# Performance work log

Hardware: AMD Instinct MI355X
Metric: run time of the kernel (lower is better)

The kernel has to match this reference:

```python
import jax, jax.numpy as jnp
import numpy as np
from jax import lax

B, N, G, K, D = 16, 8192, 256, 64, 256
DEPTH, H, HID, PH = 4, 8, 1024, 128
EPS = 1e-5
BN_SCALE = float(1.0 / np.sqrt(1.0 + 1e-5))  # BatchNorm eval, running mean 0 / var 1


def setup_inputs() -> dict:
    key = jax.random.key(0)
    ks = iter(jax.random.split(key, 48))
    def rn(shape, s=0.02):
        return jax.random.normal(next(ks), shape, jnp.float32) * s
    z = lambda *s: jnp.zeros(s, jnp.float32)
    o = lambda *s: jnp.ones(s, jnp.float32)
    return dict(
        x=jax.random.normal(next(ks), (B, N, 3), jnp.float32),
        enc_w1=rn((3, 128)), enc_b1=z(128), enc_bn1_g=o(128), enc_bn1_b=z(128),
        enc_w2=rn((128, 256)), enc_b2=z(256),
        enc_w3=rn((512, 512)), enc_b3=z(512), enc_bn2_g=o(512), enc_bn2_b=z(512),
        enc_w4=rn((512, D)), enc_b4=z(D),
        cls_token=rn((1, 1, D)), cls_pos=rn((1, 1, D)),
        pos_w1=rn((3, 128)), pos_b1=z(128), pos_w2=rn((128, D)), pos_b2=z(D),
        ln1_g=o(DEPTH, D), ln1_b=z(DEPTH, D),
        qkv_w=rn((DEPTH, D, 3 * D)),
        proj_w=rn((DEPTH, D, D)), proj_b=z(DEPTH, D),
        ln2_g=o(DEPTH, D), ln2_b=z(DEPTH, D),
        fc1_w=rn((DEPTH, D, HID)), fc1_b=z(DEPTH, HID),
        fc2_w=rn((DEPTH, HID, D)), fc2_b=z(DEPTH, D),
        norm_g=o(D), norm_b=z(D),
        head_w1=rn((D + 3, PH)), head_b1=z(PH), head_w2=rn((PH, 1)), head_b2=z(1),
    )


def layernorm(t, g, b):
    m = jnp.mean(t, -1, keepdims=True)
    v = jnp.mean((t - m) ** 2, -1, keepdims=True)
    return (t - m) / jnp.sqrt(v + EPS) * g + b


def fps(xyz, num_group):
    # farthest point sampling; deterministic start at index 0 (torch uses randint)
    Bb, Nn, _ = xyz.shape
    def body(i, st):
        dist, far, idxs = st
        idxs = idxs.at[:, i].set(far)
        cen = jnp.take_along_axis(xyz, far[:, None, None], axis=1)  # (B,1,3)
        d = jnp.sum((xyz - cen) ** 2, -1)
        dist = jnp.minimum(dist, d)
        far = jnp.argmax(dist, axis=1).astype(jnp.int32)
        return (dist, far, idxs)
    st0 = (jnp.full((Bb, Nn), 1e10, jnp.float32),
           jnp.zeros((Bb,), jnp.int32),
           jnp.zeros((Bb, num_group), jnp.int32))
    _, _, idxs = lax.fori_loop(0, num_group, body, st0)
    centers = jnp.take_along_axis(xyz, idxs[..., None], axis=1)  # (B,G,3)
    return centers, idxs


def knn(xyz, centers, k):
    # squared-distance cdist (same argsort order as p=2) + topk smallest
    c2 = jnp.sum(centers ** 2, -1)[:, :, None]
    x2 = jnp.sum(xyz ** 2, -1)[:, None, :]
    d2 = c2 + x2 - 2.0 * jnp.einsum('bgd,bnd->bgn', centers, xyz)  # (B,G,N)
    idx = lax.top_k(-d2, k)[1]  # (B,G,k)
    neigh = jax.vmap(lambda p, i: p[i])(xyz, idx)  # (B,G,k,3)
    return idx, neigh


def _forward(x, enc_w1, enc_b1, enc_bn1_g, enc_bn1_b, enc_w2, enc_b2,
             enc_w3, enc_b3, enc_bn2_g, enc_bn2_b, enc_w4, enc_b4,
             cls_token, cls_pos, pos_w1, pos_b1, pos_w2, pos_b2,
             ln1_g, ln1_b, qkv_w, proj_w, proj_b, ln2_g, ln2_b,
             fc1_w, fc1_b, fc2_w, fc2_b, norm_g, norm_b,
             head_w1, head_b1, head_w2, head_b2):
    Bb, Nn, _ = x.shape
    # grouping is @torch.no_grad() in the original -> stop_gradient
    pts = lax.stop_gradient(x)
    centers, _ = fps(pts, G)
    idx, neigh = knn(pts, centers, K)
    neigh = neigh - centers[:, :, None, :]  # (B,G,K,3) centered

    # PointNet encoder (kernel-size-1 convs == matmuls; BN eval with unit stats)
    pg = neigh.reshape(Bb * G, K, 3)
    h = pg @ enc_w1 + enc_b1                                # (BG,K,128)
    h = jax.nn.relu(h * enc_bn1_g * BN_SCALE + enc_bn1_b)
    h = h @ enc_w2 + enc_b2                                 # (BG,K,256)
    gmax = jnp.max(h, axis=1, keepdims=True)                # (BG,1,256)
    h = jnp.concatenate([jnp.broadcast_to(gmax, h.shape), h], -1)  # (BG,K,512)
    h = h @ enc_w3 + enc_b3
    h = jax.nn.relu(h * enc_bn2_g * BN_SCALE + enc_bn2_b)
    h = h @ enc_w4 + enc_b4                                 # (BG,K,D)
    tokens = jnp.max(h, axis=1).reshape(Bb, G, D)

    pos = jax.nn.gelu(centers @ pos_w1 + pos_b1, approximate=False) @ pos_w2 + pos_b2
    xt = jnp.concatenate([jnp.broadcast_to(cls_token, (Bb, 1, D)), tokens], 1)
    pt = jnp.concatenate([jnp.broadcast_to(cls_pos, (Bb, 1, D)), pos], 1)

    scale = (D // H) ** -0.5
    for l in range(DEPTH):
        xi = xt + pt  # pos added before every block
        h1 = layernorm(xi, ln1_g[l], ln1_b[l])
        qkv = (h1 @ qkv_w[l]).reshape(Bb, G + 1, 3, H, D // H).transpose(2, 0, 3, 1, 4)
        q, k_, v = qkv[0], qkv[1], qkv[2]
        attn = jax.nn.softmax(jnp.einsum('bhnd,bhmd->bhnm', q, k_) * scale, -1)
        o = jnp.einsum('bhnm,bhmd->bhnd', attn, v).transpose(0, 2, 1, 3).reshape(Bb, G + 1, D)
        xi = xi + o @ proj_w[l] + proj_b[l]
        h2 = layernorm(xi, ln2_g[l], ln2_b[l])
        xi = xi + jax.nn.gelu(h2 @ fc1_w[l] + fc1_b[l], approximate=False) @ fc2_w[l] + fc2_b[l]
        xt = xi
    xt = layernorm(xt, norm_g, norm_b)

    gfeat = xt[:, 1:, :]  # (B,G,D)
    concat = jnp.concatenate(
        [jnp.broadcast_to(gfeat[:, :, None, :], (Bb, G, K, D)), neigh], -1)  # (B,G,K,D+3)
    lg = (jax.nn.relu(concat @ head_w1 + head_b1) @ head_w2 + head_b2)[..., 0]  # (B,G,K)

    # scatter-mean per-point logits over original N points
    flat_i = idx.reshape(Bb, G * K)
    flat_v = lg.reshape(Bb, G * K)
    sums = jax.vmap(lambda v, i: jax.ops.segment_sum(v, i, num_segments=N))(flat_v, flat_i)
    cnts = jax.vmap(lambda i: jax.ops.segment_sum(jnp.ones(i.shape, jnp.float32), i, num_segments=N))(flat_i)
    return sums / jnp.maximum(cnts, 1.0)  # (B,N)


def reference(x, enc_w1, enc_b1, enc_bn1_g, enc_bn1_b, enc_w2, enc_b2,
              enc_w3, enc_b3, enc_bn2_g, enc_bn2_b, enc_w4, enc_b4,
              cls_token, cls_pos, pos_w1, pos_b1, pos_w2, pos_b2,
              ln1_g, ln1_b, qkv_w, proj_w, proj_b, ln2_g, ln2_b,
              fc1_w, fc1_b, fc2_w, fc2_b, norm_g, norm_b,
              head_w1, head_b1, head_w2, head_b2):
    return _forward(x, enc_w1, enc_b1, enc_bn1_g, enc_bn1_b, enc_w2, enc_b2,
                    enc_w3, enc_b3, enc_bn2_g, enc_bn2_b, enc_w4, enc_b4,
                    cls_token, cls_pos, pos_w1, pos_b1, pos_w2, pos_b2,
                    ln1_g, ln1_b, qkv_w, proj_w, proj_b, ln2_g, ln2_b,
                    fc1_w, fc1_b, fc2_w, fc2_b, norm_g, norm_b,
                    head_w1, head_b1, head_w2, head_b2)
```

## Files before the change

### kernel.cpp

```cpp
#include <hip/hip_runtime.h>
#include <hip/hip_bf16.h>

#define B_ 16
#define N_ 8192
#define G_ 256
#define K_ 64
#define D_ 256
#define HID_ 1024
#define EPS_ 1e-5f

typedef __attribute__((ext_vector_type(8))) short bf16x8;
typedef __attribute__((ext_vector_type(4))) float f32x4;

__device__ __forceinline__ float bf16_to_f32(unsigned short u){
  unsigned int v = ((unsigned int)u) << 16;
  return __uint_as_float(v);
}
__device__ __forceinline__ unsigned short f32_to_bf16(float f){
  unsigned int u = __float_as_uint(f);
  unsigned int r = (u + 0x7FFFu + ((u >> 16) & 1u)) >> 16;
  return (unsigned short)r;
}
__device__ __forceinline__ unsigned short bf16h(float a){
  __hip_bfloat16 h = __float2bfloat16(a);
  union { __hip_bfloat16 h; unsigned short u; } cv; cv.h = h; return cv.u;
}
__device__ __forceinline__ float gelu_exact(float v){
  return 0.5f * v * (1.0f + erff(v * 0.70710678118654752440f));
}

template<int CTRL>
__device__ __forceinline__ unsigned long long dpp64(unsigned long long k){
  int lo = (int)(unsigned int)k;
  int hi = (int)(unsigned int)(k >> 32);
  int dlo = __builtin_amdgcn_update_dpp(lo, lo, CTRL, 0xF, 0xF, false);
  int dhi = __builtin_amdgcn_update_dpp(hi, hi, CTRL, 0xF, 0xF, false);
  return (((unsigned long long)(unsigned int)dhi) << 32) | (unsigned int)dlo;
}
__device__ __forceinline__ unsigned long long bcast64(unsigned long long k, int lane){
  unsigned int lo = (unsigned int)__builtin_amdgcn_readlane((int)(unsigned int)k, lane);
  unsigned int hi = (unsigned int)__builtin_amdgcn_readlane((int)(unsigned int)(k >> 32), lane);
  return (((unsigned long long)hi) << 32) | lo;
}
__device__ __forceinline__ unsigned long long wave_max64(unsigned long long k){
  unsigned long long t;
  t = dpp64<0x111>(k); if (t > k) k = t;
  t = dpp64<0x112>(k); if (t > k) k = t;
  t = dpp64<0x114>(k); if (t > k) k = t;
  t = dpp64<0x118>(k); if (t > k) k = t;
  t = dpp64<0x142>(k); if (t > k) k = t;
  t = dpp64<0x143>(k); if (t > k) k = t;
  return bcast64(k, 63);
}
__device__ __forceinline__ unsigned long long wave_min64(unsigned long long k){
  unsigned long long t;
  t = dpp64<0x111>(k); if (t < k) k = t;
  t = dpp64<0x112>(k); if (t < k) k = t;
  t = dpp64<0x114>(k); if (t < k) k = t;
  t = dpp64<0x118>(k); if (t < k) k = t;
  t = dpp64<0x142>(k); if (t < k) k = t;
  t = dpp64<0x143>(k); if (t < k) k = t;
  return bcast64(k, 63);
}
__device__ __forceinline__ unsigned long long red8_max64(unsigned long long k){
  unsigned long long t;
  t = dpp64<0x111>(k); if (t > k) k = t;
  t = dpp64<0x112>(k); if (t > k) k = t;
  t = dpp64<0x114>(k); if (t > k) k = t;
  return bcast64(k, 7);
}
__device__ __forceinline__ unsigned long long red4_min64(unsigned long long k){
  unsigned long long t;
  t = dpp64<0x111>(k); if (t < k) k = t;
  t = dpp64<0x112>(k); if (t < k) k = t;
  return bcast64(k, 3);
}

__device__ __forceinline__ void packHi(const float* __restrict__ W, unsigned short* __restrict__ hi,
                                       int f, int N, int ksBits){
  int j = f & 7, lane = (f >> 3) & 63;
  int ks = (f >> 9) & ((1 << ksBits) - 1);
  int nt = f >> (9 + ksBits);
  int k = ks * 32 + ((lane >> 4) & 3) * 8 + j, c = nt * 16 + (lane & 15);
  hi[f] = f32_to_bf16(W[(size_t)k * N + c]);
}

__global__ __launch_bounds__(512) void prep_fps_kernel(
    const float* __restrict__ x, float* __restrict__ centers,
    const float* __restrict__ w1, const float* __restrict__ b1,
    const float* __restrict__ g1, const float* __restrict__ bb1,
    const float* __restrict__ w3, const float* __restrict__ b3,
    const float* __restrict__ g2, const float* __restrict__ bb2,
    const float* __restrict__ enc_w2, const float* __restrict__ enc_w4,
    const float* __restrict__ qkv_w, const float* __restrict__ proj_w,
    const float* __restrict__ fc1_w, const float* __restrict__ fc2_w,
    float* __restrict__ w1f, float* __restrict__ b1f, float* __restrict__ b3f,
    unsigned short* __restrict__ w2ph, unsigned short* __restrict__ w2pl,
    unsigned short* __restrict__ w3ph, unsigned short* __restrict__ w4ph,
    unsigned short* __restrict__ qkvPh, unsigned short* __restrict__ projPh,
    unsigned short* __restrict__ fc1Ph, unsigned short* __restrict__ fc2Ph,
    unsigned short* __restrict__ w3tp)
{
  const float S = 0.99999500003749968f;
  int blk = blockIdx.x, tid = threadIdx.x;

  if (blk >= 17){
    int f = (blk - 17) * 512 + tid;
    if (f < 32768){
      int j = f & 7, lane = (f >> 3) & 63, ks = (f >> 9) & 3, nt = f >> 11;
      int k = ks * 32 + ((lane >> 4) & 3) * 8 + j, c = nt * 16 + (lane & 15);
      float v = enc_w2[(size_t)k * 256 + c];
      unsigned short h = f32_to_bf16(v);
      w2ph[f] = h; w2pl[f] = f32_to_bf16(v - bf16_to_f32(h));
    } else if (f < 163840){
      f -= 32768;
      int j = f & 7, lane = (f >> 3) & 63, ks = (f >> 9) & 7, nt = f >> 12;
      int k = ks * 32 + ((lane >> 4) & 3) * 8 + j, c = nt * 16 + (lane & 15);
      w3ph[f] = f32_to_bf16(w3[(size_t)(256 + k) * 512 + c] * g2[c] * S);
    } else if (f < 294912){
      f -= 163840;
      packHi(enc_w4, w4ph, f, 256, 4);
    } else if (f < 1081344){
      f -= 294912;
      int l = f / 196608, fl = f - l * 196608;
      packHi(qkv_w + (size_t)l * 196608, qkvPh + (size_t)l * 196608, fl, 768, 3);
    } else if (f < 1343488){
      f -= 1081344;
      int l = f >> 16, fl = f & 65535;
      packHi(proj_w + (size_t)l * 65536, projPh + (size_t)l * 65536, fl, 256, 3);
    } else if (f < 2392064){
      f -= 1343488;
      int l = f >> 18, fl = f & 262143;
      packHi(fc1_w + (size_t)l * 262144, fc1Ph + (size_t)l * 262144, fl, 1024, 3);
    } else if (f < 3440640){
      f -= 2392064;
      int l = f >> 18, fl = f & 262143;
      packHi(fc2_w + (size_t)l * 262144, fc2Ph + (size_t)l * 262144, fl, 256, 5);
    } else {
      f -= 3440640;
      int j = f & 7, lane = (f >> 3) & 63, ks = (f >> 9) & 7, nt = f >> 12;
      int k = ks * 32 + ((lane >> 4) & 3) * 8 + j, c = nt * 16 + (lane & 15);
      w3tp[f] = f32_to_bf16(w3[(size_t)k * 512 + c] * g2[c] * S);
    }
    return;
  }
  if (blk == 16){
    if (tid < 384) w1f[tid] = w1[tid] * g1[tid & 127] * S;
    if (tid < 128) b1f[tid] = b1[tid] * g1[tid] * S + bb1[tid];
    b3f[tid] = b3[tid] * g2[tid] * S + bb2[tid];
    return;
  }

  int b = blk;
  const float* xb = x + (size_t)b * N_ * 3;
  int lane = tid & 63, wave = tid >> 6;
  float px[16], py[16], pz[16], dist[16];
#pragma unroll
  for (int j = 0; j < 16; j++){
    int p = tid + j * 512;
    px[j] = xb[p*3+0]; py[j] = xb[p*3+1]; pz[j] = xb[p*3+2];
    dist[j] = 1e10f;
  }
  __shared__ unsigned long long slotK[2][8];
  __shared__ float4 slotC[2][8];
  float cx = xb[0], cy = xb[1], cz = xb[2];
  for (int i = 0; i < G_; i++){
    if (tid == 0){
      float* cp = centers + ((size_t)b * G_ + i) * 3;
      cp[0] = cx; cp[1] = cy; cp[2] = cz;
    }
    float bestv = -1.0f; int bestj = 0;
#pragma unroll
    for (int j = 0; j < 16; j++){
      float dx = __fadd_rn(px[j], -cx);
      float dy = __fadd_rn(py[j], -cy);
      float dz = __fadd_rn(pz[j], -cz);
      float d  = __fadd_rn(__fadd_rn(__fmul_rn(dx,dx), __fmul_rn(dy,dy)), __fmul_rn(dz,dz));
      float dm = fminf(dist[j], d);
      dist[j] = dm;
      if (dm > bestv){ bestv = dm; bestj = j; }
    }
    unsigned int pid = (unsigned int)(tid + bestj * 512);
    unsigned long long key = (((unsigned long long)__float_as_uint(bestv)) << 32) | (unsigned long long)(~pid);
    key = wave_max64(key);
    int par = i & 1;
    unsigned int wpid = ~(unsigned int)key;
    if (lane == (int)(wpid & 63)){
      int jj = (int)(wpid >> 9);
      float fx = px[0], fy = py[0], fz = pz[0];
#pragma unroll
      for (int j = 1; j < 16; j++) if (jj == j){ fx = px[j]; fy = py[j]; fz = pz[j]; }
      slotK[par][wave] = key;
      slotC[par][wave] = make_float4(fx, fy, fz, 0.0f);
    }
    __syncthreads();
    if (i + 1 < G_){
      int sl = lane & 7;
      unsigned long long k2 = slotK[par][sl];
      float4 cc4 = slotC[par][sl];
      k2 = red8_max64(k2);
      unsigned int gpid = ~(unsigned int)k2;
      int s = (int)((gpid & 511u) >> 6);
      cx = __uint_as_float((unsigned int)__builtin_amdgcn_readlane((int)__float_as_uint(cc4.x), s));
      cy = __uint_as_float((unsigned int)__builtin_amdgcn_readlane((int)__float_as_uint(cc4.y), s));
      cz = __uint_as_float((unsigned int)__builtin_amdgcn_readlane((int)__float_as_uint(cc4.z), s));
    }
  }
}

__global__ __launch_bounds__(256) void knn_kernel(const float* __restrict__ x, const float* __restrict__ centers,
                                                  int* __restrict__ knn_idx, float* __restrict__ neigh)
{
  int blk = blockIdx.x, b = blk >> 8;
  const float* xb = x + (size_t)b * N_ * 3;
  const float* cc = centers + (size_t)blk * 3;
  int tid = threadIdx.x, lane = tid & 63, wave = tid >> 6;
  float c0 = cc[0], c1 = cc[1], c2v = cc[2];
  float c2s = __fadd_rn(__fadd_rn(__fmul_rn(c0,c0), __fmul_rn(c1,c1)), __fmul_rn(c2v,c2v));
  float d[32];
#pragma unroll
  for (int j = 0; j < 32; j++){
    int p = tid + j * 256;
    float x0 = xb[p*3+0], x1 = xb[p*3+1], x2 = xb[p*3+2];
    float xs = __fadd_rn(__fadd_rn(__fmul_rn(x0,x0), __fmul_rn(x1,x1)), __fmul_rn(x2,x2));
    float dt = __fadd_rn(__fadd_rn(__fmul_rn(c0,x0), __fmul_rn(c1,x1)), __fmul_rn(c2v,x2));
    d[j] = __fadd_rn(__fadd_rn(c2s, xs), -__fmul_rn(2.0f, dt));
  }
  const float FINF = __int_as_float(0x7F800000);
  float lmin = FINF; unsigned int lp = 0xFFFFFFFFu;
#pragma unroll
  for (int j = 0; j < 32; j++){ if (d[j] < lmin){ lmin = d[j]; lp = (unsigned int)(tid + j*256); } }
  __shared__ unsigned long long wred[2][4];
  for (int r = 0; r < K_; r++){
    unsigned int u = __float_as_uint(lmin);
    u = (u & 0x80000000u) ? ~u : (u | 0x80000000u);
    unsigned long long key = (((unsigned long long)u) << 32) | (unsigned long long)lp;
    key = wave_min64(key);
    int cur = r & 1;
    if (lane == 0) wred[cur][wave] = key;
    __syncthreads();
    unsigned long long m = red4_min64(wred[cur][lane & 3]);
    unsigned int p = (unsigned int)(m & 0xFFFFFFFFull);
    if (tid == (p & 255u)){
      knn_idx[(size_t)blk * K_ + r] = (int)p;
      float* np_ = neigh + ((size_t)blk * K_ + r) * 3;
      np_[0] = __fadd_rn(xb[p*3+0], -c0);
      np_[1] = __fadd_rn(xb[p*3+1], -c1);
      np_[2] = __fadd_rn(xb[p*3+2], -c2v);
      lmin = FINF; lp = 0xFFFFFFFFu;
#pragma unroll
      for (int j = 0; j < 32; j++){
        if ((unsigned int)(tid + j*256) == p) d[j] = FINF;
        if (d[j] < lmin){ lmin = d[j]; lp = (unsigned int)(tid + j*256); }
      }
    }
  }
}

__global__ __launch_bounds__(256, 2) void encoder_kernel(
    const float* __restrict__ neigh,
    const float* __restrict__ w1f, const float* __restrict__ b1f,
    const unsigned short* __restrict__ w2ph, const unsigned short* __restrict__ w2pl,
    const float* __restrict__ b2,
    const float* __restrict__ b3f,
    const unsigned short* __restrict__ w3ph, const unsigned short* __restrict__ w3tp,
    const unsigned short* __restrict__ w4ph,
    const float* __restrict__ b4,
    float* __restrict__ tokens)
{
  __shared__ __align__(16) unsigned short sH1[64 * 136];
  __shared__ __align__(16) unsigned short sH2[64 * 264];
  __shared__ __align__(16) float sShared[256];
  float (*sNeigh)[4] = (float(*)[4])sShared;
  unsigned short* sGmaxBf = (unsigned short*)sShared;

  int tid  = threadIdx.x;
  int wave = tid >> 6, lane = tid & 63, quad = lane >> 4, lrow = lane & 15;
  size_t gid = blockIdx.x;

  if (tid < 192) sNeigh[tid / 3][tid % 3] = neigh[gid * 192 + tid];
  __syncthreads();

  for (int e = tid; e < 8192; e += 256){
    int r = e >> 7, c = e & 127;
    float v = fmaf(sNeigh[r][2], w1f[256 + c], fmaf(sNeigh[r][1], w1f[128 + c], fmaf(sNeigh[r][0], w1f[c], b1f[c])));
    sH1[r * 136 + c] = bf16h(fmaxf(v, 0.0f));
  }
  __syncthreads();

  {
    f32x4 acc[4][4];
    const f32x4 z = {0.f, 0.f, 0.f, 0.f};
#pragma unroll
    for (int mt = 0; mt < 4; mt++)
#pragma unroll
      for (int nl = 0; nl < 4; nl++) acc[mt][nl] = z;
#pragma unroll
    for (int ks = 0; ks < 4; ks++){
      bf16x8 af[4];
#pragma unroll
      for (int mt = 0; mt < 4; mt++)
        af[mt] = *(const bf16x8*)&sH1[(mt*16 + lrow)*136 + ks*32 + quad*8];
#pragma unroll
      for (int nl = 0; nl < 4; nl++){
        size_t bo = (((size_t)(wave*4 + nl)*4 + ks)*64 + lane)*8;
        bf16x8 bh = *(const bf16x8*)&w2ph[bo];
        bf16x8 bl = *(const bf16x8*)&w2pl[bo];
#pragma unroll
        for (int mt = 0; mt < 4; mt++){
          acc[mt][nl] = __builtin_amdgcn_mfma_f32_16x16x32_bf16(af[mt], bh, acc[mt][nl], 0, 0, 0);
          acc[mt][nl] = __builtin_amdgcn_mfma_f32_16x16x32_bf16(af[mt], bl, acc[mt][nl], 0, 0, 0);
        }
      }
    }
#pragma unroll
    for (int nl = 0; nl < 4; nl++){
      int col = wave*64 + nl*16 + lrow;
      float bias = b2[col];
#pragma unroll
      for (int mt = 0; mt < 4; mt++)
#pragma unroll
        for (int rg = 0; rg < 4; rg++)
          sH2[(mt*16 + quad*4 + rg)*264 + col] = bf16h(acc[mt][nl][rg] + bias);
    }
  }
  __syncthreads();

  {
    float mx = -3.4e38f;
#pragma unroll 8
    for (int r = 0; r < 64; r++) mx = fmaxf(mx, bf16_to_f32(sH2[r*264 + tid]));
    sGmaxBf[tid] = bf16h(mx);
  }
  __syncthreads();

  f32x4 acc4[4][4];
  {
    const f32x4 z = {0.f, 0.f, 0.f, 0.f};
#pragma unroll
    for (int mt = 0; mt < 4; mt++)
#pragma unroll
      for (int nl = 0; nl < 4; nl++) acc4[mt][nl] = z;
  }
  for (int cc = 0; cc < 4; cc++){
    f32x4 acc3[4][2], accg[2];
    {
      const f32x4 z = {0.f, 0.f, 0.f, 0.f};
#pragma unroll
      for (int mt = 0; mt < 4; mt++){ acc3[mt][0] = z; acc3[mt][1] = z; }
      accg[0] = z; accg[1] = z;
    }
#pragma unroll
    for (int ks = 0; ks < 8; ks++){
      bf16x8 gf = *(const bf16x8*)&sGmaxBf[ks*32 + quad*8];
#pragma unroll
      for (int nl = 0; nl < 2; nl++){
        int nt = cc*8 + wave*2 + nl;
        size_t bo = (((size_t)nt*8 + ks)*64 + lane)*8;
        bf16x8 bh = *(const bf16x8*)&w3tp[bo];
        accg[nl] = __builtin_amdgcn_mfma_f32_16x16x32_bf16(gf, bh, accg[nl], 0, 0, 0);
      }
    }
#pragma unroll
    for (int ks = 0; ks < 8; ks++){
      bf16x8 af[4];
#pragma unroll
      for (int mt = 0; mt < 4; mt++)
        af[mt] = *(const bf16x8*)&sH2[(mt*16 + lrow)*264 + ks*32 + quad*8];
#pragma unroll
      for (int nl = 0; nl < 2; nl++){
        int nt = cc*8 + wave*2 + nl;
        size_t bo = (((size_t)nt*8 + ks)*64 + lane)*8;
        bf16x8 bh = *(const bf16x8*)&w3ph[bo];
#pragma unroll
        for (int mt = 0; mt < 4; mt++)
          acc3[mt][nl] = __builtin_amdgcn_mfma_f32_16x16x32_bf16(af[mt], bh, acc3[mt][nl], 0, 0, 0);
      }
    }
    __syncthreads();
#pragma unroll
    for (int nl = 0; nl < 2; nl++){
      int cl = wave*32 + nl*16 + lrow;
      int c  = cc*128 + cl;
      float bb = b3f[c];
#pragma unroll
      for (int mt = 0; mt < 4; mt++)
#pragma unroll
        for (int rg = 0; rg < 4; rg++)
          sH1[(mt*16 + quad*4 + rg)*136 + cl] = bf16h(fmaxf(acc3[mt][nl][rg] + accg[nl][rg] + bb, 0.0f));
    }
    __syncthreads();
#pragma unroll
    for (int ks = 0; ks < 4; ks++){
      bf16x8 af[4];
#pragma unroll
      for (int mt = 0; mt < 4; mt++)
        af[mt] = *(const bf16x8*)&sH1[(mt*16 + lrow)*136 + ks*32 + quad*8];
#pragma unroll
      for (int nl = 0; nl < 4; nl++){
        int nt = wave*4 + nl;
        size_t bo = (((size_t)nt*16 + cc*4 + ks)*64 + lane)*8;
        bf16x8 bh = *(const bf16x8*)&w4ph[bo];
#pragma unroll
        for (int mt = 0; mt < 4; mt++)
          acc4[mt][nl] = __builtin_amdgcn_mfma_f32_16x16x32_bf16(af[mt], bh, acc4[mt][nl], 0, 0, 0);
      }
    }
  }

#pragma unroll
  for (int nl = 0; nl < 4; nl++){
    float mx = -3.4e38f;
#pragma unroll
    for (int mt = 0; mt < 4; mt++)
#pragma unroll
      for (int rg = 0; rg < 4; rg++) mx = fmaxf(mx, acc4[mt][nl][rg]);
    mx = fmaxf(mx, __shfl_xor(mx, 16));
    mx = fmaxf(mx, __shfl_xor(mx, 32));
    if (quad == 0){
      int col = wave*64 + nl*16 + lrow;
      tokens[gid * 256 + col] = mx + b4[col];
    }
  }
}

__global__ __launch_bounds__(128) void pos_ln_kernel(
    const float* __restrict__ centers, const float* __restrict__ tokens,
    const float* __restrict__ cls_token, const float* __restrict__ cls_pos,
    const float* __restrict__ pw1, const float* __restrict__ pb1,
    const float* __restrict__ pw2, const float* __restrict__ pb2,
    const float* __restrict__ lng, const float* __restrict__ lnb,
    float* __restrict__ pt, float* __restrict__ xi, unsigned short* __restrict__ lnbuf)
{
  __shared__ float hS[128];
  __shared__ float red[2][2];
  int row = blockIdx.x;
  int b = row / 257, n = row - b * 257;
  int tid = threadIdx.x;
  size_t ro = (size_t)row * 256;
  float u0, u1;
  if (n == 0){
    float p0 = cls_pos[tid], p1 = cls_pos[128 + tid];
    u0 = cls_token[tid] + p0; u1 = cls_token[128 + tid] + p1;
    pt[ro + tid] = p0; pt[ro + 128 + tid] = p1;
  } else {
    int g = n - 1;
    const float* c = centers + ((size_t)b * 256 + g) * 3;
    float h = fmaf(c[2], pw1[256 + tid], fmaf(c[1], pw1[128 + tid], fmaf(c[0], pw1[tid], pb1[tid])));
    hS[tid] = gelu_exact(h);
    __syncthreads();
    const float* tok = tokens + ((size_t)b * 256 + g) * 256;
    float s0 = pb2[tid], s1 = pb2[128 + tid];
#pragma unroll 4
    for (int k = 0; k < 128; k++){
      s0 = fmaf(hS[k], pw2[(size_t)k * 256 + tid], s0);
      s1 = fmaf(hS[k], pw2[(size_t)k * 256 + 128 + tid], s1);
    }
    pt[ro + tid] = s0; pt[ro + 128 + tid] = s1;
    u0 = tok[tid] + s0; u1 = tok[128 + tid] + s1;
  }
  float s = u0 + u1, q = u0*u0 + u1*u1;
#pragma unroll
  for (int o = 32; o; o >>= 1){ s += __shfl_down(s, o); q += __shfl_down(q, o); }
  int wv = tid >> 6;
  if ((tid & 63) == 0){ red[0][wv] = s; red[1][wv] = q; }
  __syncthreads();
  float m  = (red[0][0] + red[0][1]) * (1.0f / 256.0f);
  float var = (red[1][0] + red[1][1]) * (1.0f / 256.0f) - m * m;
  float rs = 1.0f / sqrtf(var + EPS_);
  xi[ro + tid] = u0; xi[ro + 128 + tid] = u1;
  lnbuf[ro + tid] = bf16h((u0 - m) * rs * lng[tid] + lnb[tid]);
  lnbuf[ro + 128 + tid] = bf16h((u1 - m) * rs * lng[128 + tid] + lnb[128 + tid]);
}

template<int ACT>
__global__ __launch_bounds__(256) void mfma_gemm(
    const unsigned short* __restrict__ A, const unsigned short* __restrict__ Bh,
    const float* __restrict__ bias, unsigned short* __restrict__ C, int M, int K, int N)
{
  __shared__ __align__(16) unsigned short sA[64 * 72];
  int tid = threadIdx.x;
  int wave = tid >> 6, lane = tid & 63, quad = lane >> 4, lrow = lane & 15;
  int row0 = blockIdx.x * 64;
  int col0 = blockIdx.y * 128;
  int ksTotal = K >> 5;
  f32x4 acc[4][2];
  const f32x4 z = {0.f, 0.f, 0.f, 0.f};
#pragma unroll
  for (int mt = 0; mt < 4; mt++){ acc[mt][0] = z; acc[mt][1] = z; }

  for (int k0 = 0; k0 < K; k0 += 64){
#pragma unroll
    for (int i = 0; i < 2; i++){
      int e = tid + i * 256;
      int r = e >> 3, c8 = (e & 7) * 8;
      int gr = row0 + r;
      bf16x8 v = {0,0,0,0,0,0,0,0};
      if (gr < M) v = *(const bf16x8*)(A + (size_t)gr * K + k0 + c8);
      *(bf16x8*)&sA[r * 72 + c8] = v;
    }
    __syncthreads();
    int ksBase = k0 >> 5;
#pragma unroll
    for (int ks = 0; ks < 2; ks++){
      bf16x8 af[4];
#pragma unroll
      for (int mt = 0; mt < 4; mt++)
        af[mt] = *(const bf16x8*)&sA[(mt*16 + lrow)*72 + ks*32 + quad*8];
#pragma unroll
      for (int nl = 0; nl < 2; nl++){
        int nt = (col0 >> 4) + wave*2 + nl;
        size_t bo = (((size_t)nt * ksTotal + ksBase + ks)*64 + lane)*8;
        bf16x8 bh = *(const bf16x8*)&Bh[bo];
#pragma unroll
        for (int mt = 0; mt < 4; mt++)
          acc[mt][nl] = __builtin_amdgcn_mfma_f32_16x16x32_bf16(af[mt], bh, acc[mt][nl], 0, 0, 0);
      }
    }
    __syncthreads();
  }
#pragma unroll
  for (int nl = 0; nl < 2; nl++){
    int c = col0 + wave*32 + nl*16 + lrow;
    float bc = bias ? bias[c] : 0.0f;
#pragma unroll
    for (int mt = 0; mt < 4; mt++)
#pragma unroll
      for (int rg = 0; rg < 4; rg++){
        int r = row0 + mt*16 + quad*4 + rg;
        if (r < M){
          float v = acc[mt][nl][rg] + bc;
          if (ACT == 1) v = gelu_exact(v);
          C[(size_t)r * N + c] = bf16h(v);
        }
      }
  }
}

__global__ __launch_bounds__(256) void mfma_gemm_ln(
    const unsigned short* __restrict__ A, const unsigned short* __restrict__ Bh,
    const float* __restrict__ bias, const float* __restrict__ res,
    const float* __restrict__ ptb,
    float* __restrict__ C, float* __restrict__ xiOut, unsigned short* __restrict__ lnOut,
    const float* __restrict__ lng, const float* __restrict__ lnb, int M, int K)
{
  __shared__ __align__(16) unsigned short sA[64 * 72];
  __shared__ float sRed[2][64][4];
  int tid = threadIdx.x;
  int wave = tid >> 6, lane = tid & 63, quad = lane >> 4, lrow = lane & 15;
  int row0 = blockIdx.x * 64;
  int ksTotal = K >> 5;
  f32x4 acc[4][4];
  const f32x4 z = {0.f, 0.f, 0.f, 0.f};
#pragma unroll
  for (int mt = 0; mt < 4; mt++)
#pragma unroll
    for (int nl = 0; nl < 4; nl++) acc[mt][nl] = z;

  for (int k0 = 0; k0 < K; k0 += 64){
#pragma unroll
    for (int i = 0; i < 2; i++){
      int e = tid + i * 256;
      int r = e >> 3, c8 = (e & 7) * 8;
      int gr = row0 + r;
      bf16x8 v = {0,0,0,0,0,0,0,0};
      if (gr < M) v = *(const bf16x8*)(A + (size_t)gr * K + k0 + c8);
      *(bf16x8*)&sA[r * 72 + c8] = v;
    }
    __syncthreads();
    int ksBase = k0 >> 5;
#pragma unroll
    for (int ks = 0; ks < 2; ks++){
      bf16x8 af[4];
#pragma unroll
      for (int mt = 0; mt < 4; mt++)
        af[mt] = *(const bf16x8*)&sA[(mt*16 + lrow)*72 + ks*32 + quad*8];
#pragma unroll
      for (int nl = 0; nl < 4; nl++){
        int nt = wave*4 + nl;
        size_t bo = (((size_t)nt * ksTotal + ksBase + ks)*64 + lane)*8;
        bf16x8 bh = *(const bf16x8*)&Bh[bo];
#pragma unroll
        for (int mt = 0; mt < 4; mt++)
          acc[mt][nl] = __builtin_amdgcn_mfma_f32_16x16x32_bf16(af[mt], bh, acc[mt][nl], 0, 0, 0);
      }
    }
    __syncthreads();
  }
#pragma unroll
  for (int nl = 0; nl < 4; nl++){
    int c = wave*64 + nl*16 + lrow;
    float bc = bias[c];
#pragma unroll
    for (int mt = 0; mt < 4; mt++)
#pragma unroll
      for (int rg = 0; rg < 4; rg++){
        int r = row0 + mt*16 + quad*4 + rg;
        if (r < M){
          float v = acc[mt][nl][rg] + bc + res[(size_t)r * 256 + c];
          if (C) C[(size_t)r * 256 + c] = v;
          float u = v;
          if (ptb) u += ptb[(size_t)r * 256 + c];
          acc[mt][nl][rg] = u;
        }
      }
  }
#pragma unroll
  for (int mt = 0; mt < 4; mt++)
#pragma unroll
    for (int rg = 0; rg < 4; rg++){
      int rloc = mt*16 + quad*4 + rg;
      float s = 0.0f, q = 0.0f;
#pragma unroll
      for (int nl = 0; nl < 4; nl++){ float u = acc[mt][nl][rg]; s += u; q += u*u; }
#pragma unroll
      for (int off = 1; off < 16; off <<= 1){ s += __shfl_xor(s, off); q += __shfl_xor(q, off); }
      if (lrow == 0){ sRed[0][rloc][wave] = s; sRed[1][rloc][wave] = q; }
    }
  __syncthreads();
#pragma unroll
  for (int mt = 0; mt < 4; mt++)
#pragma unroll
    for (int rg = 0; rg < 4; rg++){
      int rloc = mt*16 + quad*4 + rg;
      int r = row0 + rloc;
      if (r >= M) continue;
      float s = ((sRed[0][rloc][0] + sRed[0][rloc][1]) + sRed[0][rloc][2]) + sRed[0][rloc][3];
      float q = ((sRed[1][rloc][0] + sRed[1][rloc][1]) + sRed[1][rloc][2]) + sRed[1][rloc][3];
      float m  = s * (1.0f / 256.0f);
      float var = q * (1.0f / 256.0f) - m * m;
      float rs = 1.0f / sqrtf(var + EPS_);
#pragma unroll
      for (int nl = 0; nl < 4; nl++){
        int c = wave*64 + nl*16 + lrow;
        float u = acc[mt][nl][rg];
        lnOut[(size_t)r * 256 + c] = bf16h((u - m) * rs * lng[c] + lnb[c]);
        if (xiOut) xiOut[(size_t)r * 256 + c] = u;
      }
    }
}

__global__ __launch_bounds__(256) void attn_kernel(const unsigned short* __restrict__ qkv, unsigned short* __restrict__ obuf)
{
  int bh = blockIdx.x;
  int b = bh >> 3, h = bh & 7;
  int tid = threadIdx.x;
  int qi = tid >> 2, kp = tid & 3;
  int qrow = blockIdx.y * 64 + qi;
  bool act = qrow < 257;
  __shared__ float kS[128][33];
  __shared__ float vS[128][33];
  const unsigned short* qb = qkv + (size_t)b * 257 * 768;
  float q[32], o[32];
  float mrun = -3.4e38f, l = 0.0f;
  if (act){
    const unsigned short* qr = qb + (size_t)qrow * 768 + h * 32;
#pragma unroll
    for (int j = 0; j < 32; j++){ q[j] = bf16_to_f32(qr[j]); o[j] = 0.0f; }
  }
  const float scale = 0.17677669529663687f;
  for (int m0 = 0; m0 < 257; m0 += 128){
    int cnt = min(128, 257 - m0);
    for (int e = tid; e < cnt * 32; e += 256){
      int mm = e >> 5, j = e & 31;
      const unsigned short* rowp = qb + (size_t)(m0 + mm) * 768 + h * 32;
      kS[mm][j] = bf16_to_f32(rowp[256 + j]);
      vS[mm][j] = bf16_to_f32(rowp[512 + j]);
    }
    __syncthreads();
    if (act){
      for (int mm = kp; mm < cnt; mm += 4){
        float s = 0.0f;
#pragma unroll
        for (int j = 0; j < 32; j++) s = fmaf(q[j], kS[mm][j], s);
        s *= scale;
        float nm = fmaxf(mrun, s);
        float alpha = expf(mrun - nm);
        float p = expf(s - nm);
        l = fmaf(l, alpha, p);
#pragma unroll
        for (int j = 0; j < 32; j++) o[j] = fmaf(p, vS[mm][j], o[j] * alpha);
        mrun = nm;
      }
    }
    __syncthreads();
  }
  if (act){
#pragma unroll
    for (int msk = 1; msk <= 2; msk <<= 1){
      float m2 = __shfl_xor(mrun, msk);
      float l2 = __shfl_xor(l, msk);
      float nm = fmaxf(mrun, m2);
      float a1 = expf(mrun - nm), a2 = expf(m2 - nm);
      l = l * a1 + l2 * a2;
#pragma unroll
      for (int j = 0; j < 32; j++){
        float o2 = __shfl_xor(o[j], msk);
        o[j] = o[j] * a1 + o2 * a2;
      }
      mrun = nm;
    }
    if (kp == 0){
      float inv = 1.0f / l;
      unsigned short* orow = obuf + (size_t)(b * 257 + qrow) * 256 + h * 32;
#pragma unroll
      for (int j = 0; j < 32; j++) orow[j] = bf16h(o[j] * inv);
    }
  }
}

__global__ __launch_bounds__(256) void head_kernel(
    const unsigned short* __restrict__ gfeat, const float* __restrict__ neigh, const int* __restrict__ knn_idx,
    const float* __restrict__ w1, const float* __restrict__ b1,
    const float* __restrict__ w2, const float* __restrict__ b2,
    float* __restrict__ sums, float* __restrict__ cnts)
{
  int blk = blockIdx.x, b = blk >> 8;
  __shared__ float xS[256];
  __shared__ float nS[64][4];
  __shared__ float partH[2][128];
  __shared__ float sharedH[128];
  __shared__ float w2S[128];
  __shared__ float wtail[3][128];
  int tid = threadIdx.x;
  xS[tid] = bf16_to_f32(gfeat[((size_t)b * 257 + 1 + (blk & 255)) * 256 + tid]);
  if (tid < 192) nS[tid / 3][tid % 3] = neigh[(size_t)blk * 192 + tid];
  if (tid < 128){
    w2S[tid] = w2[tid];
    wtail[0][tid] = w1[256 * 128 + tid];
    wtail[1][tid] = w1[257 * 128 + tid];
    wtail[2][tid] = w1[258 * 128 + tid];
  }
  __syncthreads();
  {
    int half = tid >> 7, j = tid & 127;
    float s = 0.0f;
#pragma unroll 8
    for (int k = 0; k < 128; k++) s = fmaf(xS[half * 128 + k], w1[(size_t)(half * 128 + k) * 128 + j], s);
    partH[half][j] = s;
  }
  __syncthreads();
  if (tid < 128) sharedH[tid] = partH[0][tid] + partH[1][tid] + b1[tid];
  __syncthreads();
  int r = tid >> 2, q = tid & 3;
  float n0 = nS[r][0], n1 = nS[r][1], n2 = nS[r][2];
  float s = 0.0f;
#pragma unroll
  for (int j0 = 0; j0 < 32; j0++){
    int j = q * 32 + j0;
    float h = fmaf(n2, wtail[2][j], fmaf(n1, wtail[1][j], fmaf(n0, wtail[0][j], sharedH[j])));
    s = fmaf(fmaxf(h, 0.0f), w2S[j], s);
  }
  s += __shfl_xor(s, 1);
  s += __shfl_xor(s, 2);
  if (q == 0){
    float lg = s + b2[0];
    int p = knn_idx[(size_t)blk * K_ + r];
    atomicAdd(&sums[(size_t)b * N_ + p], lg);
    atomicAdd(&cnts[(size_t)b * N_ + p], 1.0f);
  }
}

__global__ void finalize_kernel(const float* __restrict__ sums, const float* __restrict__ cnts, float* __restrict__ out)
{
  int i = blockIdx.x * 256 + threadIdx.x;
  out[i] = sums[i] / fmaxf(cnts[i], 1.0f);
}

extern "C" void kernel_launch(void* const* d_in, const int* in_sizes, int n_in,
                              void* d_out, int out_size, void* d_ws, size_t ws_size,
                              hipStream_t stream)
{
  (void)in_sizes; (void)n_in; (void)out_size; (void)ws_size;
  const float* x        = (const float*)d_in[0];
  const float* enc_w1   = (const float*)d_in[1];
  const float* enc_b1   = (const float*)d_in[2];
  const float* enc_bn1g = (const float*)d_in[3];
  const float* enc_bn1b = (const float*)d_in[4];
  const float* enc_w2   = (const float*)d_in[5];
  const float* enc_b2   = (const float*)d_in[6];
  const float* enc_w3   = (const float*)d_in[7];
  const float* enc_b3   = (const float*)d_in[8];
  const float* enc_bn2g = (const float*)d_in[9];
  const float* enc_bn2b = (const float*)d_in[10];
  const float* enc_w4   = (const float*)d_in[11];
  const float* enc_b4   = (const float*)d_in[12];
  const float* cls_tok  = (const float*)d_in[13];
  const float* cls_pos  = (const float*)d_in[14];
  const float* pos_w1   = (const float*)d_in[15];
  const float* pos_b1   = (const float*)d_in[16];
  const float* pos_w2   = (const float*)d_in[17];
  const float* pos_b2   = (const float*)d_in[18];
  const float* ln1_g    = (const float*)d_in[19];
  const float* ln1_b    = (const float*)d_in[20];
  const float* qkv_w    = (const float*)d_in[21];
  const float* proj_w   = (const float*)d_in[22];
  const float* proj_b   = (const float*)d_in[23];
  const float* ln2_g    = (const float*)d_in[24];
  const float* ln2_b    = (const float*)d_in[25];
  const float* fc1_w    = (const float*)d_in[26];
  const float* fc1_b    = (const float*)d_in[27];
  const float* fc2_w    = (const float*)d_in[28];
  const float* fc2_b    = (const float*)d_in[29];
  const float* norm_g   = (const float*)d_in[30];
  const float* norm_b   = (const float*)d_in[31];
  const float* head_w1  = (const float*)d_in[32];
  const float* head_b1  = (const float*)d_in[33];
  const float* head_w2  = (const float*)d_in[34];
  const float* head_b2  = (const float*)d_in[35];

  float* ws = (float*)d_ws;
  size_t off = 0;
  auto alloc = [&](size_t n)->float*{ float* p = ws + off; off += (n + 63) & ~(size_t)63; return p; };

  float* centers = alloc((size_t)B_ * G_ * 3);
  float* w1f     = alloc(384);
  float* b1f     = alloc(128);
  float* b3f     = alloc(512);
  unsigned short* w2ph = (unsigned short*)alloc(16384);
  unsigned short* w2pl = (unsigned short*)alloc(16384);
  unsigned short* w3ph = (unsigned short*)alloc(65536);
  unsigned short* w3tp = (unsigned short*)alloc(65536);
  unsigned short* w4ph = (unsigned short*)alloc(65536);
  unsigned short* qkvPh = (unsigned short*)alloc(393216);
  unsigned short* projPh = (unsigned short*)alloc(131072);
  unsigned short* fc1Ph = (unsigned short*)alloc(524288);
  unsigned short* fc2Ph = (unsigned short*)alloc(524288);
  float* tokens  = alloc((size_t)B_ * G_ * D_);
  float* neigh   = alloc((size_t)B_ * G_ * K_ * 3);
  int*   knn_idx = (int*)alloc((size_t)B_ * G_ * K_);
  float* pt      = alloc((size_t)B_ * 257 * D_);
  float* xi      = alloc((size_t)B_ * 257 * D_);
  unsigned short* lnbufB = (unsigned short*)alloc((size_t)B_ * 257 * D_ / 2 + 64);
  unsigned short* obufB  = (unsigned short*)alloc((size_t)B_ * 257 * D_ / 2 + 64);
  unsigned short* bigbufB= (unsigned short*)alloc((size_t)B_ * 257 * HID_ / 2 + 64);
  unsigned short* gfeatB = (unsigned short*)alloc((size_t)B_ * 257 * D_ / 2 + 64);
  float* sums    = alloc((size_t)B_ * N_);
  float* cnts    = alloc((size_t)B_ * N_);

  hipMemsetAsync(sums, 0, (size_t)2 * B_ * N_ * sizeof(float), stream);

  prep_fps_kernel<<<6993, 512, 0, stream>>>(x, centers,
      enc_w1, enc_b1, enc_bn1g, enc_bn1b, enc_w3, enc_b3, enc_bn2g, enc_bn2b,
      enc_w2, enc_w4, qkv_w, proj_w, fc1_w, fc2_w,
      w1f, b1f, b3f, w2ph, w2pl, w3ph, w4ph, qkvPh, projPh, fc1Ph, fc2Ph, w3tp);

  knn_kernel<<<B_ * G_, 256, 0, stream>>>(x, centers, knn_idx, neigh);
  encoder_kernel<<<B_ * G_, 256, 0, stream>>>(neigh, w1f, b1f, w2ph, w2pl, enc_b2,
                                              b3f, w3ph, w3tp, w4ph, enc_b4, tokens);
  pos_ln_kernel<<<B_ * 257, 128, 0, stream>>>(centers, tokens, cls_tok, cls_pos,
                                              pos_w1, pos_b1, pos_w2, pos_b2,
                                              ln1_g, ln1_b, pt, xi, lnbufB);
  const int M = B_ * 257;
  for (int l = 0; l < 4; l++){
    mfma_gemm<0><<<dim3(65, 6), 256, 0, stream>>>(lnbufB, qkvPh + (size_t)l*196608, nullptr, bigbufB, M, 256, 768);
    attn_kernel<<<dim3(B_ * 8, 5), 256, 0, stream>>>(bigbufB, obufB);
    mfma_gemm_ln<<<65, 256, 0, stream>>>(obufB, projPh + (size_t)l*65536, proj_b + l*256, xi, nullptr,
                                         xi, nullptr, lnbufB, ln2_g + l*256, ln2_b + l*256, M, 256);
    mfma_gemm<1><<<dim3(65, 8), 256, 0, stream>>>(lnbufB, fc1Ph + (size_t)l*262144, fc1_b + l*1024, bigbufB, M, 256, 1024);
    if (l < 3){
      mfma_gemm_ln<<<65, 256, 0, stream>>>(bigbufB, fc2Ph + (size_t)l*262144, fc2_b + l*256, xi, pt,
                                           nullptr, xi, lnbufB, ln1_g + (l+1)*256, ln1_b + (l+1)*256, M, 1024);
    } else {
      mfma_gemm_ln<<<65, 256, 0, stream>>>(bigbufB, fc2Ph + (size_t)l*262144, fc2_b + l*256, xi, nullptr,
                                           nullptr, nullptr, gfeatB, norm_g, norm_b, M, 1024);
    }
  }
  head_kernel<<<B_ * G_, 256, 0, stream>>>(gfeatB, neigh, knn_idx, head_w1, head_b1, head_w2, head_b2, sums, cnts);
  finalize_kernel<<<(B_ * N_) / 256, 256, 0, stream>>>(sums, cnts, (float*)d_out);
}
```

Baseline: 1.814 ms.

## Buffer FPS/KNN outputs in LDS and shrink GEMM row tiles for more blocks

FPS centers and KNN indices/neighbour offsets are now staged in shared memory and written to global memory in one coalesced pass at kernel end, instead of scattered single-thread stores inside the serial loops. The transformer GEMMs shrink their row tile from 64 to 32 rows (plain GEMM) and to 16 rows (GEMM+LayerNorm), which multiplies the grid size so the M≈4112 problem fills more compute units. The smaller tiles reduce weight reuse per block and increase redundant B-operand loads.

```diff
diff --git a/kernel.cpp b/kernel.cpp
--- a/kernel.cpp
+++ b/kernel.cpp
@@ -163,11 +163,11 @@
   }
   __shared__ unsigned long long slotK[2][8];
   __shared__ float4 slotC[2][8];
+  __shared__ float sCen[G_ * 3];
   float cx = xb[0], cy = xb[1], cz = xb[2];
   for (int i = 0; i < G_; i++){
     if (tid == 0){
-      float* cp = centers + ((size_t)b * G_ + i) * 3;
-      cp[0] = cx; cp[1] = cy; cp[2] = cz;
+      sCen[i*3+0] = cx; sCen[i*3+1] = cy; sCen[i*3+2] = cz;
     }
     float bestv = -1.0f; int bestj = 0;
 #pragma unroll
@@ -206,6 +206,9 @@
       cz = __uint_as_float((unsigned int)__builtin_amdgcn_readlane((int)__float_as_uint(cc4.z), s));
     }
   }
+  __syncthreads();
+  for (int e = tid; e < G_ * 3; e += 512)
+    centers[(size_t)b * G_ * 3 + e] = sCen[e];
 }
 
 __global__ __launch_bounds__(256) void knn_kernel(const float* __restrict__ x, const float* __restrict__ centers,
@@ -231,6 +234,8 @@
 #pragma unroll
   for (int j = 0; j < 32; j++){ if (d[j] < lmin){ lmin = d[j]; lp = (unsigned int)(tid + j*256); } }
   __shared__ unsigned long long wred[2][4];
+  __shared__ int sIdx[K_];
+  __shared__ float sNei[K_ * 3];
   for (int r = 0; r < K_; r++){
     unsigned int u = __float_as_uint(lmin);
     u = (u & 0x80000000u) ? ~u : (u | 0x80000000u);
@@ -242,11 +247,10 @@
     unsigned long long m = red4_min64(wred[cur][lane & 3]);
     unsigned int p = (unsigned int)(m & 0xFFFFFFFFull);
     if (tid == (p & 255u)){
-      knn_idx[(size_t)blk * K_ + r] = (int)p;
-      float* np_ = neigh + ((size_t)blk * K_ + r) * 3;
-      np_[0] = __fadd_rn(xb[p*3+0], -c0);
-      np_[1] = __fadd_rn(xb[p*3+1], -c1);
-      np_[2] = __fadd_rn(xb[p*3+2], -c2v);
+      sIdx[r] = (int)p;
+      sNei[r*3+0] = __fadd_rn(xb[p*3+0], -c0);
+      sNei[r*3+1] = __fadd_rn(xb[p*3+1], -c1);
+      sNei[r*3+2] = __fadd_rn(xb[p*3+2], -c2v);
       lmin = FINF; lp = 0xFFFFFFFFu;
 #pragma unroll
       for (int j = 0; j < 32; j++){
@@ -255,6 +259,9 @@
       }
     }
   }
+  __syncthreads();
+  if (tid < K_) knn_idx[(size_t)blk * K_ + tid] = sIdx[tid];
+  if (tid < K_ * 3) neigh[(size_t)blk * K_ * 3 + tid] = sNei[tid];
 }
 
 __global__ __launch_bounds__(256, 2) void encoder_kernel(
@@ -478,22 +485,20 @@
     const unsigned short* __restrict__ A, const unsigned short* __restrict__ Bh,
     const float* __restrict__ bias, unsigned short* __restrict__ C, int M, int K, int N)
 {
-  __shared__ __align__(16) unsigned short sA[64 * 72];
+  __shared__ __align__(16) unsigned short sA[32 * 72];
   int tid = threadIdx.x;
   int wave = tid >> 6, lane = tid & 63, quad = lane >> 4, lrow = lane & 15;
-  int row0 = blockIdx.x * 64;
+  int row0 = blockIdx.x * 32;
   int col0 = blockIdx.y * 128;
   int ksTotal = K >> 5;
-  f32x4 acc[4][2];
+  f32x4 acc[2][2];
   const f32x4 z = {0.f, 0.f, 0.f, 0.f};
 #pragma unroll
-  for (int mt = 0; mt < 4; mt++){ acc[mt][0] = z; acc[mt][1] = z; }
+  for (int mt = 0; mt < 2; mt++){ acc[mt][0] = z; acc[mt][1] = z; }
 
   for (int k0 = 0; k0 < K; k0 += 64){
-#pragma unroll
-    for (int i = 0; i < 2; i++){
-      int e = tid + i * 256;
-      int r = e >> 3, c8 = (e & 7) * 8;
+    {
+      int r = tid >> 3, c8 = (tid & 7) * 8;
       int gr = row0 + r;
       bf16x8 v = {0,0,0,0,0,0,0,0};
       if (gr < M) v = *(const bf16x8*)(A + (size_t)gr * K + k0 + c8);
@@ -503,9 +508,9 @@
     int ksBase = k0 >> 5;
 #pragma unroll
     for (int ks = 0; ks < 2; ks++){
-      bf16x8 af[4];
-#pragma unroll
-      for (int mt = 0; mt < 4; mt++)
+      bf16x8 af[2];
+#pragma unroll
+      for (int mt = 0; mt < 2; mt++)
         af[mt] = *(const bf16x8*)&sA[(mt*16 + lrow)*72 + ks*32 + quad*8];
 #pragma unroll
       for (int nl = 0; nl < 2; nl++){
@@ -513,7 +518,7 @@
         size_t bo = (((size_t)nt * ksTotal + ksBase + ks)*64 + lane)*8;
         bf16x8 bh = *(const bf16x8*)&Bh[bo];
 #pragma unroll
-        for (int mt = 0; mt < 4; mt++)
+        for (int mt = 0; mt < 2; mt++)
           acc[mt][nl] = __builtin_amdgcn_mfma_f32_16x16x32_bf16(af[mt], bh, acc[mt][nl], 0, 0, 0);
       }
     }
@@ -524,7 +529,7 @@
     int c = col0 + wave*32 + nl*16 + lrow;
     float bc = bias ? bias[c] : 0.0f;
 #pragma unroll
-    for (int mt = 0; mt < 4; mt++)
+    for (int mt = 0; mt < 2; mt++)
 #pragma unroll
       for (int rg = 0; rg < 4; rg++){
         int r = row0 + mt*16 + quad*4 + rg;
@@ -544,24 +549,20 @@
     float* __restrict__ C, float* __restrict__ xiOut, unsigned short* __restrict__ lnOut,
     const float* __restrict__ lng, const float* __restrict__ lnb, int M, int K)
 {
-  __shared__ __align__(16) unsigned short sA[64 * 72];
-  __shared__ float sRed[2][64][4];
+  __shared__ __align__(16) unsigned short sA[16 * 72];
+  __shared__ float sRed[2][16][4];
   int tid = threadIdx.x;
   int wave = tid >> 6, lane = tid & 63, quad = lane >> 4, lrow = lane & 15;
-  int row0 = blockIdx.x * 64;
+  int row0 = blockIdx.x * 16;
   int ksTotal = K >> 5;
-  f32x4 acc[4][4];
+  f32x4 acc[4];
   const f32x4 z = {0.f, 0.f, 0.f, 0.f};
 #pragma unroll
-  for (int mt = 0; mt < 4; mt++)
-#pragma unroll
-    for (int nl = 0; nl < 4; nl++) acc[mt][nl] = z;
+  for (int nl = 0; nl < 4; nl++) acc[nl] = z;
 
   for (int k0 = 0; k0 < K; k0 += 64){
-#pragma unroll
-    for (int i = 0; i < 2; i++){
-      int e = tid + i * 256;
-      int r = e >> 3, c8 = (e & 7) * 8;
+    if (tid < 128){
+      int r = tid >> 3, c8 = (tid & 7) * 8;
       int gr = row0 + r;
       bf16x8 v = {0,0,0,0,0,0,0,0};
       if (gr < M) v = *(const bf16x8*)(A + (size_t)gr * K + k0 + c8);
@@ -571,18 +572,13 @@
     int ksBase = k0 >> 5;
 #pragma unroll
     for (int ks = 0; ks < 2; ks++){
-      bf16x8 af[4];
-#pragma unroll
-      for (int mt = 0; mt < 4; mt++)
-        af[mt] = *(const bf16x8*)&sA[(mt*16 + lrow)*72 + ks*32 + quad*8];
+      bf16x8 af = *(const bf16x8*)&sA[lrow*72 + ks*32 + quad*8];
 #pragma unroll
       for (int nl = 0; nl < 4; nl++){
         int nt = wave*4 + nl;
         size_t bo = (((size_t)nt * ksTotal + ksBase + ks)*64 + lane)*8;
         bf16x8 bh = *(const bf16x8*)&Bh[bo];
-#pragma unroll
-        for (int mt = 0; mt < 4; mt++)
-          acc[mt][nl] = __builtin_amdgcn_mfma_f32_16x16x32_bf16(af[mt], bh, acc[mt][nl], 0, 0, 0);
+        acc[nl] = __builtin_amdgcn_mfma_f32_16x16x32_bf16(af, bh, acc[nl], 0, 0, 0);
       }
     }
     __syncthreads();
@@ -592,52 +588,46 @@
     int c = wave*64 + nl*16 + lrow;
     float bc = bias[c];
 #pragma unroll
-    for (int mt = 0; mt < 4; mt++)
-#pragma unroll
-      for (int rg = 0; rg < 4; rg++){
-        int r = row0 + mt*16 + quad*4 + rg;
-        if (r < M){
-          float v = acc[mt][nl][rg] + bc + res[(size_t)r * 256 + c];
-          if (C) C[(size_t)r * 256 + c] = v;
-          float u = v;
-          if (ptb) u += ptb[(size_t)r * 256 + c];
-          acc[mt][nl][rg] = u;
-        }
-      }
-  }
-#pragma unroll
-  for (int mt = 0; mt < 4; mt++)
-#pragma unroll
     for (int rg = 0; rg < 4; rg++){
-      int rloc = mt*16 + quad*4 + rg;
-      float s = 0.0f, q = 0.0f;
-#pragma unroll
-      for (int nl = 0; nl < 4; nl++){ float u = acc[mt][nl][rg]; s += u; q += u*u; }
-#pragma unroll
-      for (int off = 1; off < 16; off <<= 1){ s += __shfl_xor(s, off); q += __shfl_xor(q, off); }
-      if (lrow == 0){ sRed[0][rloc][wave] = s; sRed[1][rloc][wave] = q; }
-    }
-  __syncthreads();
-#pragma unroll
-  for (int mt = 0; mt < 4; mt++)
-#pragma unroll
-    for (int rg = 0; rg < 4; rg++){
-      int rloc = mt*16 + quad*4 + rg;
-      int r = row0 + rloc;
-      if (r >= M) continue;
-      float s = ((sRed[0][rloc][0] + sRed[0][rloc][1]) + sRed[0][rloc][2]) + sRed[0][rloc][3];
-      float q = ((sRed[1][rloc][0] + sRed[1][rloc][1]) + sRed[1][rloc][2]) + sRed[1][rloc][3];
-      float m  = s * (1.0f / 256.0f);
-      float var = q * (1.0f / 256.0f) - m * m;
-      float rs = 1.0f / sqrtf(var + EPS_);
-#pragma unroll
-      for (int nl = 0; nl < 4; nl++){
-        int c = wave*64 + nl*16 + lrow;
-        float u = acc[mt][nl][rg];
-        lnOut[(size_t)r * 256 + c] = bf16h((u - m) * rs * lng[c] + lnb[c]);
-        if (xiOut) xiOut[(size_t)r * 256 + c] = u;
-      }
-    }
+      int r = row0 + quad*4 + rg;
+      if (r < M){
+        float v = acc[nl][rg] + bc + res[(size_t)r * 256 + c];
+        if (C) C[(size_t)r * 256 + c] = v;
+        float u = v;
+        if (ptb) u += ptb[(size_t)r * 256 + c];
+        acc[nl][rg] = u;
+      }
+    }
+  }
+#pragma unroll
+  for (int rg = 0; rg < 4; rg++){
+    int rloc = quad*4 + rg;
+    float s = 0.0f, q = 0.0f;
+#pragma unroll
+    for (int nl = 0; nl < 4; nl++){ float u = acc[nl][rg]; s += u; q += u*u; }
+#pragma unroll
+    for (int off = 1; off < 16; off <<= 1){ s += __shfl_xor(s, off); q += __shfl_xor(q, off); }
+    if (lrow == 0){ sRed[0][rloc][wave] = s; sRed[1][rloc][wave] = q; }
+  }
+  __syncthreads();
+#pragma unroll
+  for (int rg = 0; rg < 4; rg++){
+    int rloc = quad*4 + rg;
+    int r = row0 + rloc;
+    if (r >= M) continue;
+    float s = ((sRed[0][rloc][0] + sRed[0][rloc][1]) + sRed[0][rloc][2]) + sRed[0][rloc][3];
+    float q = ((sRed[1][rloc][0] + sRed[1][rloc][1]) + sRed[1][rloc][2]) + sRed[1][rloc][3];
+    float m  = s * (1.0f / 256.0f);
+    float var = q * (1.0f / 256.0f) - m * m;
+    float rs = 1.0f / sqrtf(var + EPS_);
+#pragma unroll
+    for (int nl = 0; nl < 4; nl++){
+      int c = wave*64 + nl*16 + lrow;
+      float u = acc[nl][rg];
+      lnOut[(size_t)r * 256 + c] = bf16h((u - m) * rs * lng[c] + lnb[c]);
+      if (xiOut) xiOut[(size_t)r * 256 + c] = u;
+    }
+  }
 }
 
 __global__ __launch_bounds__(256) void attn_kernel(const unsigned short* __restrict__ qkv, unsigned short* __restrict__ obuf)
@@ -853,17 +843,17 @@
                                               ln1_g, ln1_b, pt, xi, lnbufB);
   const int M = B_ * 257;
   for (int l = 0; l < 4; l++){
-    mfma_gemm<0><<<dim3(65, 6), 256, 0, stream>>>(lnbufB, qkvPh + (size_t)l*196608, nullptr, bigbufB, M, 256, 768);
+    mfma_gemm<0><<<dim3(129, 6), 256, 0, stream>>>(lnbufB, qkvPh + (size_t)l*196608, nullptr, bigbufB, M, 256, 768);
     attn_kernel<<<dim3(B_ * 8, 5), 256, 0, stream>>>(bigbufB, obufB);
-    mfma_gemm_ln<<<65, 256, 0, stream>>>(obufB, projPh + (size_t)l*65536, proj_b + l*256, xi, nullptr,
-                                         xi, nullptr, lnbufB, ln2_g + l*256, ln2_b + l*256, M, 256);
-    mfma_gemm<1><<<dim3(65, 8), 256, 0, stream>>>(lnbufB, fc1Ph + (size_t)l*262144, fc1_b + l*1024, bigbufB, M, 256, 1024);
+    mfma_gemm_ln<<<257, 256, 0, stream>>>(obufB, projPh + (size_t)l*65536, proj_b + l*256, xi, nullptr,
+                                          xi, nullptr, lnbufB, ln2_g + l*256, ln2_b + l*256, M, 256);
+    mfma_gemm<1><<<dim3(129, 8), 256, 0, stream>>>(lnbufB, fc1Ph + (size_t)l*262144, fc1_b + l*1024, bigbufB, M, 256, 1024);
     if (l < 3){
-      mfma_gemm_ln<<<65, 256, 0, stream>>>(bigbufB, fc2Ph + (size_t)l*262144, fc2_b + l*256, xi, pt,
-                                           nullptr, xi, lnbufB, ln1_g + (l+1)*256, ln1_b + (l+1)*256, M, 1024);
+      mfma_gemm_ln<<<257, 256, 0, stream>>>(bigbufB, fc2Ph + (size_t)l*262144, fc2_b + l*256, xi, pt,
+                                            nullptr, xi, lnbufB, ln1_g + (l+1)*256, ln1_b + (l+1)*256, M, 1024);
     } else {
-      mfma_gemm_ln<<<65, 256, 0, stream>>>(bigbufB, fc2Ph + (size_t)l*262144, fc2_b + l*256, xi, nullptr,
-                                           nullptr, nullptr, gfeatB, norm_g, norm_b, M, 1024);
+      mfma_gemm_ln<<<257, 256, 0, stream>>>(bigbufB, fc2Ph + (size_t)l*262144, fc2_b + l*256, xi, nullptr,
+                                            nullptr, nullptr, gfeatB, norm_g, norm_b, M, 1024);
     }
   }
   head_kernel<<<B_ * G_, 256, 0, stream>>>(gfeatB, neigh, knn_idx, head_w1, head_b1, head_w2, head_b2, sums, cnts);
```

After: 1.650 ms. 9.1% less time.
